# Kernel optimization log

Measured on AMD Instinct MI355X. Metric: run time of the kernel, lower is better.

Reference implementation:

```python
import jax, jax.numpy as jnp
import numpy as np

N, E, F_IN, H, G, A, OUT = 50000, 800000, 128, 256, 64, 8, 1


def _lin(k, fi, fo):
    s = 1.0 / np.sqrt(fi)
    kw, kb = jax.random.split(k)
    W = jax.random.uniform(kw, (fi, fo), jnp.float32, -s, s)
    b = jax.random.uniform(kb, (fo,), jnp.float32, -s, s)
    return W, b


def setup_inputs() -> dict:
    key = jax.random.key(0)
    ks = jax.random.split(key, 12)
    x = jax.random.normal(ks[0], (N, F_IN), jnp.float32)
    edge_index = jax.random.randint(ks[1], (2, E), 0, N, dtype=jnp.int64)
    batch = jnp.sort(jax.random.randint(ks[2], (N,), 0, G, dtype=jnp.int64))
    graph_attr = jax.random.normal(ks[3], (G, A), jnp.float32)
    W1, b1 = _lin(ks[4], F_IN, H)
    W2, b2 = _lin(ks[5], H, H)
    W3, b3 = _lin(ks[6], H, H)
    fcW1, fcb1 = _lin(ks[7], H + A, H)
    fcW2, fcb2 = _lin(ks[8], H, OUT)
    ones = jnp.ones((H,), jnp.float32)
    zeros = jnp.zeros((H,), jnp.float32)
    return dict(x=x, graph_attr=graph_attr, edge_index=edge_index, batch=batch,
                W1=W1, b1=b1, W2=W2, b2=b2, W3=W3, b3=b3,
                g1=ones, be1=zeros, g2=ones, be2=zeros, g3=ones, be3=zeros,
                fcW1=fcW1, fcb1=fcb1, fcW2=fcW2, fcb2=fcb2)


def gcn_conv(x, W, b, src, dst, n):
    # PyG GCNConv: add self-loops, symmetric normalization, xW then scatter-add
    xw = x @ W  # [N, H]
    loop = jnp.arange(n)
    src2 = jnp.concatenate([src, loop])
    dst2 = jnp.concatenate([dst, loop])
    deg = jnp.zeros((n,), xw.dtype).at[dst2].add(1.0)
    dinv = jnp.where(deg > 0, jax.lax.rsqrt(deg), 0.0)
    norm = dinv[src2] * dinv[dst2]  # [E+N]
    out = jnp.zeros((n, xw.shape[1]), xw.dtype).at[dst2].add(xw[src2] * norm[:, None])
    return out + b


def layer_norm(x, g, b, eps=1e-5):
    m = x.mean(-1, keepdims=True)
    v = ((x - m) ** 2).mean(-1, keepdims=True)
    return (x - m) * jax.lax.rsqrt(v + eps) * g + b


def reference(x, graph_attr, edge_index, batch,
              W1, b1, W2, b2, W3, b3,
              g1, be1, g2, be2, g3, be3,
              fcW1, fcb1, fcW2, fcb2):
    src, dst = edge_index[0], edge_index[1]
    h = jax.nn.relu(layer_norm(gcn_conv(x, W1, b1, src, dst, N), g1, be1))
    h = jax.nn.relu(layer_norm(gcn_conv(h, W2, b2, src, dst, N), g2, be2))
    h = jax.nn.relu(layer_norm(gcn_conv(h, W3, b3, src, dst, N), g3, be3))
    # global mean pool over graph ids
    sums = jax.ops.segment_sum(h, batch, num_segments=G)
    cnts = jax.ops.segment_sum(jnp.ones((N,), h.dtype), batch, num_segments=G)
    pooled = sums / jnp.maximum(cnts, 1.0)[:, None]  # [G, H]
    z = jnp.concatenate([pooled, graph_attr.reshape(-1, A)], axis=1)
    z = jax.nn.relu(z @ fcW1 + fcb1)
    return z @ fcW2 + fcb2  # [G, OUT]
```

## Files before the change

kernel.cpp:

```cpp
#include <hip/hip_runtime.h>
#include <hip/hip_bf16.h>

#define N_NODES 50000
#define N_EDGES 800000
#define F_IN    128
#define H_DIM   256
#define G_NUM   64
#define A_DIM   8

#define NBUCKET 196
#define NCHUNK  391
#define CHUNK   2048
#define K4CAP   6144

typedef __attribute__((ext_vector_type(8))) short short8v;
typedef __attribute__((ext_vector_type(4))) float float4v;
typedef __attribute__((ext_vector_type(2))) float float2v;

__device__ __forceinline__ float b2f(unsigned short u) {
    return __uint_as_float(((unsigned int)u) << 16);
}
__device__ __forceinline__ unsigned short f2b(float v) {
    return __hip_bfloat16_raw(__float2bfloat16(v)).x;
}
__device__ __forceinline__ unsigned char f2fp8(float v) {
    return (unsigned char)(__builtin_amdgcn_cvt_pk_fp8_f32(v, v, 0, false) & 0xff);
}
__device__ __forceinline__ unsigned int pack2(float a, float b) {
    return (unsigned int)f2b(a) | ((unsigned int)f2b(b) << 16);
}
__device__ __forceinline__ void accadd16(float2v* a, uint4 v) {
    a[0] += __builtin_amdgcn_cvt_pk_f32_fp8((int)v.x, false);
    a[1] += __builtin_amdgcn_cvt_pk_f32_fp8((int)v.x, true);
    a[2] += __builtin_amdgcn_cvt_pk_f32_fp8((int)v.y, false);
    a[3] += __builtin_amdgcn_cvt_pk_f32_fp8((int)v.y, true);
    a[4] += __builtin_amdgcn_cvt_pk_f32_fp8((int)v.z, false);
    a[5] += __builtin_amdgcn_cvt_pk_f32_fp8((int)v.z, true);
    a[6] += __builtin_amdgcn_cvt_pk_f32_fp8((int)v.w, false);
    a[7] += __builtin_amdgcn_cvt_pk_f32_fp8((int)v.w, true);
}
__device__ __forceinline__ void accfma16(float2v* a, uint4 v, float w) {
    float2v w2 = {w, w};
    a[0] = __builtin_amdgcn_cvt_pk_f32_fp8((int)v.x, false) * w2 + a[0];
    a[1] = __builtin_amdgcn_cvt_pk_f32_fp8((int)v.x, true)  * w2 + a[1];
    a[2] = __builtin_amdgcn_cvt_pk_f32_fp8((int)v.y, false) * w2 + a[2];
    a[3] = __builtin_amdgcn_cvt_pk_f32_fp8((int)v.y, true)  * w2 + a[3];
    a[4] = __builtin_amdgcn_cvt_pk_f32_fp8((int)v.z, false) * w2 + a[4];
    a[5] = __builtin_amdgcn_cvt_pk_f32_fp8((int)v.z, true)  * w2 + a[5];
    a[6] = __builtin_amdgcn_cvt_pk_f32_fp8((int)v.w, false) * w2 + a[6];
    a[7] = __builtin_amdgcn_cvt_pk_f32_fp8((int)v.w, true)  * w2 + a[7];
}

#define SK 40


__global__ __launch_bounds__(512) void fuse0_kernel(const int* __restrict__ dst,
                                                    unsigned int* __restrict__ Hg,
                                                    const float* __restrict__ x,
                                                    const float* __restrict__ W1,
                                                    unsigned char* __restrict__ P8,
                                                    const float* __restrict__ W2,
                                                    unsigned short* __restrict__ Wt2,
                                                    const float* __restrict__ W3,
                                                    unsigned short* __restrict__ Wt3) {
    const int CB = NCHUNK;
    const int GB = (N_NODES + 127) / 128;
    int b = blockIdx.x, t = threadIdx.x;
    if (b < CB) {
        __shared__ unsigned int h[256];
        if (t < 256) h[t] = 0u;
        __syncthreads();
        int base = b * CHUNK;
        #pragma unroll
        for (int k = 0; k < 4; k++) {
            int i = base + k * 512 + t;
            if (i < N_EDGES) atomicAdd(&h[dst[i] >> 8], 1u);
        }
        __syncthreads();
        if (t < 256) Hg[(size_t)t * NCHUNK + b] = h[t];
        return;
    }
    b -= CB;
    if (b < GB) {
        __shared__ unsigned short As[128][SK];
        __shared__ unsigned short Bs[256][SK];
        int wave = t >> 6, lane = t & 63;
        int wm0 = (wave & 1) * 64, wn0 = (wave >> 1) * 64;
        int bm = b * 128;
        int l15 = lane & 15, lq = lane >> 4;
        float4v acc[4][4];
        #pragma unroll
        for (int i = 0; i < 4; i++)
            #pragma unroll
            for (int j = 0; j < 4; j++)
                acc[i][j] = (float4v){0.f, 0.f, 0.f, 0.f};

        for (int k0 = 0; k0 < F_IN; k0 += 32) {
            {
                int row = t >> 2, koff = (t & 3) * 8;
                short8v tmp = (short8v){0,0,0,0,0,0,0,0};
                if (bm + row < N_NODES) {
                    const float* xp = x + (size_t)(bm + row) * F_IN + k0 + koff;
                    float4 a0 = *(const float4*)xp;
                    float4 a1 = *(const float4*)(xp + 4);
                    tmp[0] = (short)f2b(a0.x); tmp[1] = (short)f2b(a0.y);
                    tmp[2] = (short)f2b(a0.z); tmp[3] = (short)f2b(a0.w);
                    tmp[4] = (short)f2b(a1.x); tmp[5] = (short)f2b(a1.y);
                    tmp[6] = (short)f2b(a1.z); tmp[7] = (short)f2b(a1.w);
                }
                *(short8v*)&As[row][koff] = tmp;
            }
            #pragma unroll
            for (int h = 0; h < 2; h++) {
                int c = t + h * 512;
                int n = c >> 2, koff = (c & 3) * 8;
                short8v tmp;
                #pragma unroll
                for (int kk = 0; kk < 8; kk++)
                    tmp[kk] = (short)f2b(W1[(size_t)(k0 + koff + kk) * H_DIM + n]);
                *(short8v*)&Bs[n][koff] = tmp;
            }
            __syncthreads();
            short8v af[4], bf[4];
            #pragma unroll
            for (int i = 0; i < 4; i++) {
                af[i] = *(const short8v*)&As[wm0 + i * 16 + l15][lq * 8];
                bf[i] = *(const short8v*)&Bs[wn0 + i * 16 + l15][lq * 8];
            }
            #pragma unroll
            for (int i = 0; i < 4; i++)
                #pragma unroll
                for (int j = 0; j < 4; j++)
                    acc[i][j] = __builtin_amdgcn_mfma_f32_16x16x32_bf16(af[i], bf[j], acc[i][j], 0, 0, 0);
            __syncthreads();
        }
        #pragma unroll
        for (int i = 0; i < 4; i++) {
            #pragma unroll
            for (int r = 0; r < 4; r++) {
                int row = bm + wm0 + i * 16 + lq * 4 + r;
                if (row < N_NODES) {
                    #pragma unroll
                    for (int j = 0; j < 4; j++) {
                        int col = wn0 + j * 16 + l15;
                        P8[(size_t)row * H_DIM + col] = f2fp8(acc[i][j][r]);
                    }
                }
            }
        }
        return;
    }
    b -= GB;
    int i = b * 512 + t;
    if (i < H_DIM * H_DIM) {
        int k = i >> 8, n = i & 255;
        Wt2[(size_t)n * H_DIM + k] = f2b(W2[i]);
    } else if (i < 2 * H_DIM * H_DIM) {
        int j = i - H_DIM * H_DIM;
        int k = j >> 8, n = j & 255;
        Wt3[(size_t)n * H_DIM + k] = f2b(W3[j]);
    }
}


__global__ __launch_bounds__(256) void scanH_kernel(unsigned int* __restrict__ Hg,
                                                    unsigned int* __restrict__ Btot) {
    __shared__ unsigned int tile[256];
    int b = blockIdx.x, t = threadIdx.x;
    unsigned int* row = Hg + (size_t)b * NCHUNK;
    int i0 = 2 * t, i1 = 2 * t + 1;
    unsigned int v0 = (i0 < NCHUNK) ? row[i0] : 0u;
    unsigned int v1 = (i1 < NCHUNK) ? row[i1] : 0u;
    unsigned int pair = v0 + v1;
    tile[t] = pair;
    __syncthreads();
    #pragma unroll
    for (int o = 1; o < 256; o <<= 1) {
        unsigned int add = (t >= o) ? tile[t - o] : 0u;
        __syncthreads();
        tile[t] += add;
        __syncthreads();
    }
    unsigned int excl = tile[t] - pair;
    if (i0 < NCHUNK) row[i0] = excl;
    if (i1 < NCHUNK) row[i1] = excl + v0;
    if (t == 255) Btot[b] = tile[255];
}


__global__ __launch_bounds__(256) void base_kernel(const unsigned int* __restrict__ Btot,
                                                   unsigned int* __restrict__ bucketBase,
                                                   const int* __restrict__ batch,
                                                   int* __restrict__ gstart,
                                                   int* __restrict__ rowptr,
                                                   float* __restrict__ pooled) {
    __shared__ unsigned int tile[256];
    int t = threadIdx.x;
    unsigned int v = (t < NBUCKET) ? Btot[t] : 0u;
    tile[t] = v;
    __syncthreads();
    #pragma unroll
    for (int o = 1; o < 256; o <<= 1) {
        unsigned int add = (t >= o) ? tile[t - o] : 0u;
        __syncthreads();
        tile[t] += add;
        __syncthreads();
    }
    if (t < NBUCKET) bucketBase[t] = tile[t] - v;
    if (t == NBUCKET - 1) bucketBase[NBUCKET] = tile[t];
    if (t == 0) rowptr[N_NODES] = N_EDGES;
    if (t <= G_NUM) {
        int lo = 0, hi = N_NODES;
        while (lo < hi) {
            int mid = (lo + hi) >> 1;
            if (batch[mid] < t) lo = mid + 1; else hi = mid;
        }
        gstart[t] = lo;
    }
    for (int i = t; i < G_NUM * H_DIM; i += 256) pooled[i] = 0.f;
}


__global__ __launch_bounds__(512) void scatter_kernel(const int* __restrict__ src,
                                                      const int* __restrict__ dst,
                                                      const unsigned int* __restrict__ Hg,
                                                      const unsigned int* __restrict__ bucketBase,
                                                      unsigned int* __restrict__ tmp) {
    __shared__ unsigned int off[256];
    int blk = blockIdx.x, t = threadIdx.x;
    if (t < 256)
        off[t] = (t < NBUCKET) ? (bucketBase[t] + Hg[(size_t)t * NCHUNK + blk]) : 0u;
    __syncthreads();
    int base = blk * CHUNK;
    #pragma unroll
    for (int k = 0; k < 4; k++) {
        int i = base + k * 512 + t;
        if (i < N_EDGES) {
            int d = dst[i], s = src[i];
            unsigned int slot = atomicAdd(&off[d >> 8], 1u);
            tmp[slot] = ((unsigned int)(d & 255) << 16) | (unsigned int)s;
        }
    }
}


__global__ __launch_bounds__(256) void finalize_kernel(const unsigned int* __restrict__ tmp,
                                                       const unsigned int* __restrict__ bucketBase,
                                                       int* __restrict__ rowptr,
                                                       float* __restrict__ dinv,
                                                       unsigned short* __restrict__ csr_src) {
    __shared__ unsigned int te[K4CAP];
    __shared__ unsigned int h2[256];
    __shared__ unsigned int sc[256];
    __shared__ unsigned int off2[256];
    int b = blockIdx.x, t = threadIdx.x;
    unsigned int beg = bucketBase[b], end = bucketBase[b + 1];
    int cnt = (int)(end - beg);
    bool lds_ok = (cnt <= K4CAP);
    h2[t] = 0u;
    __syncthreads();
    for (int i = t; i < cnt; i += 256) {
        unsigned int u = tmp[beg + i];
        if (lds_ok) te[i] = u;
        atomicAdd(&h2[u >> 16], 1u);
    }
    __syncthreads();
    unsigned int c = h2[t];
    sc[t] = c;
    __syncthreads();
    #pragma unroll
    for (int o = 1; o < 256; o <<= 1) {
        unsigned int add = (t >= o) ? sc[t - o] : 0u;
        __syncthreads();
        sc[t] += add;
        __syncthreads();
    }
    unsigned int excl = sc[t] - c;
    int v = (b << 8) + t;
    if (v < N_NODES) {
        rowptr[v] = (int)(beg + excl);
        dinv[v] = rsqrtf((float)c + 1.0f);
    }
    off2[t] = excl;
    __syncthreads();
    for (int i = t; i < cnt; i += 256) {
        unsigned int u = lds_ok ? te[i] : tmp[beg + i];
        unsigned int lo = u >> 16;
        unsigned int s2 = atomicAdd(&off2[lo], 1u);
        csr_src[beg + s2] = (unsigned short)(u & 0xFFFFu);
    }
}


__global__ __launch_bounds__(512) void gemm_f8(const unsigned short* __restrict__ A,
                                               const unsigned short* __restrict__ Bt,
                                               unsigned char* __restrict__ C8,
                                               const float* __restrict__ dinv,
                                               int M, int K) {
    __shared__ unsigned short As[128][SK];
    __shared__ unsigned short Bs[256][SK];
    int t = threadIdx.x;
    int wave = t >> 6, lane = t & 63;
    int wm0 = (wave & 1) * 64, wn0 = (wave >> 1) * 64;
    int bm = blockIdx.x * 128;
    int l15 = lane & 15, lq = lane >> 4;
    float4v acc[4][4];
    #pragma unroll
    for (int i = 0; i < 4; i++)
        #pragma unroll
        for (int j = 0; j < 4; j++)
            acc[i][j] = (float4v){0.f, 0.f, 0.f, 0.f};

    for (int k0 = 0; k0 < K; k0 += 32) {
        {
            int row = t >> 2, koff = (t & 3) * 8;
            uint4 va = make_uint4(0u, 0u, 0u, 0u);
            if (bm + row < M)
                va = *(const uint4*)(A + (size_t)(bm + row) * K + k0 + koff);
            *(uint4*)&As[row][koff] = va;
        }
        #pragma unroll
        for (int h = 0; h < 2; h++) {
            int c = t + h * 512;
            int row = c >> 2, koff = (c & 3) * 8;
            uint4 vb = *(const uint4*)(Bt + (size_t)row * K + k0 + koff);
            *(uint4*)&Bs[row][koff] = vb;
        }
        __syncthreads();
        short8v af[4], bf[4];
        #pragma unroll
        for (int i = 0; i < 4; i++) {
            af[i] = *(const short8v*)&As[wm0 + i * 16 + l15][lq * 8];
            bf[i] = *(const short8v*)&Bs[wn0 + i * 16 + l15][lq * 8];
        }
        #pragma unroll
        for (int i = 0; i < 4; i++)
            #pragma unroll
            for (int j = 0; j < 4; j++)
                acc[i][j] = __builtin_amdgcn_mfma_f32_16x16x32_bf16(af[i], bf[j], acc[i][j], 0, 0, 0);
        __syncthreads();
    }
    #pragma unroll
    for (int i = 0; i < 4; i++) {
        #pragma unroll
        for (int r = 0; r < 4; r++) {
            int row = bm + wm0 + i * 16 + lq * 4 + r;
            if (row < M) {
                float dv = dinv[row];
                #pragma unroll
                for (int j = 0; j < 4; j++) {
                    int col = wn0 + j * 16 + l15;
                    C8[(size_t)row * H_DIM + col] = f2fp8(dv * acc[i][j][r]);
                }
            }
        }
    }
}


template<int F, bool DO_LN, bool W8>
__global__ __launch_bounds__(256) void gather_ns(const unsigned char* __restrict__ xw,
                                                 unsigned short* __restrict__ out,
                                                 const int* __restrict__ rowptr,
                                                 const unsigned short* __restrict__ csr_src,
                                                 const float* __restrict__ dinv,
                                                 const float* __restrict__ bias,
                                                 const float* __restrict__ gamma,
                                                 const float* __restrict__ beta) {
    constexpr int BPL = F / 16;
    constexpr int NF2 = BPL / 2;
    int lane = threadIdx.x & 63;
    int wave = threadIdx.x >> 6;
    int p = lane & 15;
    int gbase = lane & 48;
    int node = blockIdx.x * 16 + wave * 4 + (lane >> 4);
    int beg = rowptr[node];
    int deg = rowptr[node + 1] - beg;
    float d = dinv[node];
    const unsigned char* xp = xw + (size_t)p * BPL;

    float2v acc2[NF2];
    #pragma unroll
    for (int k = 0; k < NF2; k++) acc2[k] = (float2v){0.f, 0.f};

    {
        uint4 v = *(const uint4*)(xp + (size_t)node * F);
        if constexpr (W8) accfma16(acc2, v, d);
        else              accadd16(acc2, v);
    }

    for (int b0 = 0; b0 < deg; b0 += 16) {
        int m = deg - b0; if (m > 16) m = 16;
        int sv = 0; float wv = 0.f;
        if (p < m) {
            sv = (int)csr_src[beg + b0 + p];
            if constexpr (W8) wv = dinv[sv];
        }
        int j = 0;
        for (; j + 4 <= m; j += 4) {
            int s0 = __shfl(sv, gbase | j, 64);
            int s1 = __shfl(sv, gbase | (j + 1), 64);
            int s2 = __shfl(sv, gbase | (j + 2), 64);
            int s3 = __shfl(sv, gbase | (j + 3), 64);
            uint4 v0 = *(const uint4*)(xp + (size_t)s0 * F);
            uint4 v1 = *(const uint4*)(xp + (size_t)s1 * F);
            uint4 v2 = *(const uint4*)(xp + (size_t)s2 * F);
            uint4 v3 = *(const uint4*)(xp + (size_t)s3 * F);
            if constexpr (W8) {
                float w0 = __shfl(wv, gbase | j, 64);
                float w1 = __shfl(wv, gbase | (j + 1), 64);
                float w2 = __shfl(wv, gbase | (j + 2), 64);
                float w3 = __shfl(wv, gbase | (j + 3), 64);
                accfma16(acc2, v0, w0); accfma16(acc2, v1, w1);
                accfma16(acc2, v2, w2); accfma16(acc2, v3, w3);
            } else {
                accadd16(acc2, v0); accadd16(acc2, v1);
                accadd16(acc2, v2); accadd16(acc2, v3);
            }
        }
        for (; j < m; ++j) {
            int s0 = __shfl(sv, gbase | j, 64);
            uint4 v0 = *(const uint4*)(xp + (size_t)s0 * F);
            if constexpr (W8) {
                float w0 = __shfl(wv, gbase | j, 64);
                accfma16(acc2, v0, w0);
            } else {
                accadd16(acc2, v0);
            }
        }
    }

    float v[BPL];
    #pragma unroll
    for (int k = 0; k < NF2; k++) { v[2 * k] = d * acc2[k].x; v[2 * k + 1] = d * acc2[k].y; }

    if constexpr (DO_LN) {
        #pragma unroll
        for (int q = 0; q < BPL / 4; q++) {
            float4 bi = ((const float4*)bias)[p * (BPL / 4) + q];
            v[q * 4 + 0] += bi.x; v[q * 4 + 1] += bi.y;
            v[q * 4 + 2] += bi.z; v[q * 4 + 3] += bi.w;
        }
        float s = 0.f, ss = 0.f;
        #pragma unroll
        for (int k = 0; k < BPL; k++) { s += v[k]; ss += v[k] * v[k]; }
        #pragma unroll
        for (int o = 1; o < 16; o <<= 1) {
            s  += __shfl_xor(s, o, 64);
            ss += __shfl_xor(ss, o, 64);
        }
        float mn = s * (1.f / F);
        float var = ss * (1.f / F) - mn * mn;
        float rstd = rsqrtf(var + 1e-5f);
        #pragma unroll
        for (int q = 0; q < BPL / 4; q++) {
            float4 ga = ((const float4*)gamma)[p * (BPL / 4) + q];
            float4 be = ((const float4*)beta)[p * (BPL / 4) + q];
            v[q * 4 + 0] = fmaxf((v[q * 4 + 0] - mn) * rstd * ga.x + be.x, 0.f);
            v[q * 4 + 1] = fmaxf((v[q * 4 + 1] - mn) * rstd * ga.y + be.y, 0.f);
            v[q * 4 + 2] = fmaxf((v[q * 4 + 2] - mn) * rstd * ga.z + be.z, 0.f);
            v[q * 4 + 3] = fmaxf((v[q * 4 + 3] - mn) * rstd * ga.w + be.w, 0.f);
        }
    }

    unsigned short* op = out + (size_t)node * F + p * BPL;
    uint4 o0;
    o0.x = pack2(v[0], v[1]); o0.y = pack2(v[2], v[3]);
    o0.z = pack2(v[4], v[5]); o0.w = pack2(v[6], v[7]);
    *(uint4*)op = o0;
    if constexpr (F == 256) {
        uint4 o1;
        o1.x = pack2(v[8],  v[9]);  o1.y = pack2(v[10], v[11]);
        o1.z = pack2(v[12], v[13]); o1.w = pack2(v[14], v[15]);
        *(uint4*)(op + 8) = o1;
    }
}


__global__ __launch_bounds__(128) void pool_kernel(const unsigned int* __restrict__ h32,
                                                   const int* __restrict__ batch,
                                                   float* __restrict__ pooled, int n) {
    int t = threadIdx.x;
    int start = blockIdx.x * 64;
    int end = min(start + 64, n);
    if (start >= n) return;
    int cur = batch[start];
    float a0 = 0.f, a1 = 0.f;
    for (int i = start; i < end; ++i) {
        int g = batch[i];
        if (g != cur) {
            atomicAdd(&pooled[(size_t)cur * H_DIM + 2 * t], a0);
            atomicAdd(&pooled[(size_t)cur * H_DIM + 2 * t + 1], a1);
            a0 = a1 = 0.f;
            cur = g;
        }
        unsigned int u = h32[(size_t)i * (H_DIM / 2) + t];
        a0 += b2f((unsigned short)(u & 0xffffu));
        a1 += b2f((unsigned short)(u >> 16));
    }
    atomicAdd(&pooled[(size_t)cur * H_DIM + 2 * t], a0);
    atomicAdd(&pooled[(size_t)cur * H_DIM + 2 * t + 1], a1);
}


__global__ __launch_bounds__(256) void fc_kernel(const float* __restrict__ pooled,
                                                 const int* __restrict__ gstart,
                                                 const float* __restrict__ gattr,
                                                 const float* __restrict__ fcW1,
                                                 const float* __restrict__ fcb1,
                                                 const float* __restrict__ fcW2,
                                                 const float* __restrict__ fcb2,
                                                 float* __restrict__ out) {
    __shared__ float zc[H_DIM + A_DIM];
    __shared__ float z1[H_DIM];
    int g = blockIdx.x, t = threadIdx.x;
    int c_i = gstart[g + 1] - gstart[g];
    float c = (float)(c_i > 1 ? c_i : 1);
    zc[t] = pooled[(size_t)g * H_DIM + t] / c;
    if (t < A_DIM) zc[H_DIM + t] = gattr[g * A_DIM + t];
    __syncthreads();
    float s = fcb1[t];
    for (int k = 0; k < H_DIM + A_DIM; k++)
        s += zc[k] * fcW1[(size_t)k * H_DIM + t];
    z1[t] = fmaxf(s, 0.f) * fcW2[t];
    __syncthreads();
    for (int off = 128; off; off >>= 1) {
        if (t < off) z1[t] += z1[t + off];
        __syncthreads();
    }
    if (t == 0) out[g] = z1[0] + fcb2[0];
}


extern "C" void kernel_launch(void* const* d_in, const int* in_sizes, int n_in,
                              void* d_out, int out_size, void* d_ws, size_t ws_size,
                              hipStream_t stream) {
    const float* x     = (const float*)d_in[0];
    const float* gattr = (const float*)d_in[1];
    const int*   ei    = (const int*)d_in[2];
    const int*   batch = (const int*)d_in[3];
    const float* W1 = (const float*)d_in[4];  const float* b1 = (const float*)d_in[5];
    const float* W2 = (const float*)d_in[6];  const float* b2 = (const float*)d_in[7];
    const float* W3 = (const float*)d_in[8];  const float* b3 = (const float*)d_in[9];
    const float* g1 = (const float*)d_in[10]; const float* be1 = (const float*)d_in[11];
    const float* g2 = (const float*)d_in[12]; const float* be2 = (const float*)d_in[13];
    const float* g3 = (const float*)d_in[14]; const float* be3 = (const float*)d_in[15];
    const float* fcW1 = (const float*)d_in[16]; const float* fcb1 = (const float*)d_in[17];
    const float* fcW2 = (const float*)d_in[18]; const float* fcb2 = (const float*)d_in[19];
    float* out = (float*)d_out;

    char* w = (char*)d_ws;
    unsigned char*  Pb8 = (unsigned char*)w;  w += (size_t)N_NODES * H_DIM;
    unsigned short* Hb  = (unsigned short*)w; w += (size_t)N_NODES * H_DIM * 2;
    unsigned short* Wt2 = (unsigned short*)w; w += (size_t)H_DIM * H_DIM * 2;
    unsigned short* Wt3 = (unsigned short*)w; w += (size_t)H_DIM * H_DIM * 2;
    float* dinv   = (float*)w; w += (size_t)N_NODES * 4;
    float* pooled = (float*)w; w += (size_t)G_NUM * H_DIM * 4;
    int* rowptr   = (int*)w;   w += (size_t)(N_NODES + 4) * 4;
    unsigned int* Hg = (unsigned int*)w;      w += (size_t)256 * NCHUNK * 4;
    unsigned int* Btot = (unsigned int*)w;    w += (size_t)256 * 4;
    unsigned int* bucketBase = (unsigned int*)w; w += (size_t)(NBUCKET + 4) * 4;
    unsigned int* tmp = (unsigned int*)w;     w += (size_t)N_EDGES * 4;
    unsigned short* csr_src = (unsigned short*)w; w += (size_t)N_EDGES * 2;
    int* gstart   = (int*)w;   w += (size_t)(G_NUM + 1) * 4;

    const int* srcp = ei;
    const int* dstp = ei + N_EDGES;

    {
        const int CB = NCHUNK;
        const int GB = (N_NODES + 127) / 128;
        const int WB = (2 * H_DIM * H_DIM + 511) / 512;
        fuse0_kernel<<<CB + GB + WB, 512, 0, stream>>>(dstp, Hg, x, W1, Pb8, W2, Wt2, W3, Wt3);
    }
    scanH_kernel<<<NBUCKET, 256, 0, stream>>>(Hg, Btot);
    base_kernel<<<1, 256, 0, stream>>>(Btot, bucketBase, batch, gstart, rowptr, pooled);
    scatter_kernel<<<NCHUNK, 512, 0, stream>>>(srcp, dstp, Hg, bucketBase, tmp);
    finalize_kernel<<<NBUCKET, 256, 0, stream>>>(tmp, bucketBase, rowptr, dinv, csr_src);

    int gemm_blocks = (N_NODES + 127) / 128;
    int gather_blocks = N_NODES / 16;

    gather_ns<H_DIM, true, true><<<gather_blocks, 256, 0, stream>>>(Pb8, Hb, rowptr, csr_src,
                                                                    dinv, b1, g1, be1);
    gemm_f8<<<gemm_blocks, 512, 0, stream>>>(Hb, Wt2, Pb8, dinv, N_NODES, H_DIM);
    gather_ns<H_DIM, true, false><<<gather_blocks, 256, 0, stream>>>(Pb8, Hb, rowptr, csr_src,
                                                                     dinv, b2, g2, be2);
    gemm_f8<<<gemm_blocks, 512, 0, stream>>>(Hb, Wt3, Pb8, dinv, N_NODES, H_DIM);
    gather_ns<H_DIM, true, false><<<gather_blocks, 256, 0, stream>>>(Pb8, Hb, rowptr, csr_src,
                                                                     dinv, b3, g3, be3);

    pool_kernel<<<(N_NODES + 63) / 64, 128, 0, stream>>>((const unsigned int*)Hb, batch, pooled, N_NODES);
    fc_kernel<<<G_NUM, 256, 0, stream>>>(pooled, gstart, gattr, fcW1, fcb1, fcW2, fcb2, out);
}
```

Measured before the change: 339.3 us.

## Fuse gather+LayerNorm into the following GEMM and fuse final gather with pooling

Each aggregation+LayerNorm stage now writes its 64-row bf16 tile into swizzled shared memory, and the next layer's MFMA GEMM consumes it directly in the same kernel, writing fp8 output to a ping-pong buffer. The final aggregation is fused with mean-pool accumulation through shared-memory atomics. This removes the bf16 intermediate round-trips to global memory and several launches. In exchange, the GEMM runs with smaller 64-row tiles, reloads the weight panel in every block, and sees the gather's load imbalance.

```diff
diff --git a/kernel.cpp b/kernel.cpp
--- a/kernel.cpp
+++ b/kernel.cpp
@@ -52,6 +52,104 @@
 }
 
 #define SK 40
+
+
+template<bool W8>
+__device__ __forceinline__ void gather_row_256(const unsigned char* __restrict__ xw,
+                                               int node,
+                                               const int* __restrict__ rowptr,
+                                               const unsigned short* __restrict__ csr_src,
+                                               const float* __restrict__ dinv,
+                                               const float* __restrict__ bias,
+                                               const float* __restrict__ gamma,
+                                               const float* __restrict__ beta,
+                                               int p, int gbase, float* v) {
+    int beg = rowptr[node];
+    int deg = rowptr[node + 1] - beg;
+    float d = dinv[node];
+    const unsigned char* xp = xw + (size_t)p * 16;
+
+    float2v acc2[8];
+    #pragma unroll
+    for (int k = 0; k < 8; k++) acc2[k] = (float2v){0.f, 0.f};
+
+    {
+        uint4 sv4 = *(const uint4*)(xp + (size_t)node * H_DIM);
+        if constexpr (W8) accfma16(acc2, sv4, d);
+        else              accadd16(acc2, sv4);
+    }
+
+    for (int b0 = 0; b0 < deg; b0 += 16) {
+        int m = deg - b0; if (m > 16) m = 16;
+        int sv = 0; float wv = 0.f;
+        if (p < m) {
+            sv = (int)csr_src[beg + b0 + p];
+            if constexpr (W8) wv = dinv[sv];
+        }
+        int j = 0;
+        for (; j + 4 <= m; j += 4) {
+            int s0 = __shfl(sv, gbase | j, 64);
+            int s1 = __shfl(sv, gbase | (j + 1), 64);
+            int s2 = __shfl(sv, gbase | (j + 2), 64);
+            int s3 = __shfl(sv, gbase | (j + 3), 64);
+            uint4 v0 = *(const uint4*)(xp + (size_t)s0 * H_DIM);
+            uint4 v1 = *(const uint4*)(xp + (size_t)s1 * H_DIM);
+            uint4 v2 = *(const uint4*)(xp + (size_t)s2 * H_DIM);
+            uint4 v3 = *(const uint4*)(xp + (size_t)s3 * H_DIM);
+            if constexpr (W8) {
+                float w0 = __shfl(wv, gbase | j, 64);
+                float w1 = __shfl(wv, gbase | (j + 1), 64);
+                float w2 = __shfl(wv, gbase | (j + 2), 64);
+                float w3 = __shfl(wv, gbase | (j + 3), 64);
+                accfma16(acc2, v0, w0); accfma16(acc2, v1, w1);
+                accfma16(acc2, v2, w2); accfma16(acc2, v3, w3);
+            } else {
+                accadd16(acc2, v0); accadd16(acc2, v1);
+                accadd16(acc2, v2); accadd16(acc2, v3);
+            }
+        }
+        for (; j < m; ++j) {
+            int s0 = __shfl(sv, gbase | j, 64);
+            uint4 v0 = *(const uint4*)(xp + (size_t)s0 * H_DIM);
+            if constexpr (W8) {
+                float w0 = __shfl(wv, gbase | j, 64);
+                accfma16(acc2, v0, w0);
+            } else {
+                accadd16(acc2, v0);
+            }
+        }
+    }
+
+    #pragma unroll
+    for (int k = 0; k < 8; k++) { v[2 * k] = d * acc2[k].x; v[2 * k + 1] = d * acc2[k].y; }
+
+    #pragma unroll
+    for (int q = 0; q < 4; q++) {
+        float4 bi = ((const float4*)bias)[p * 4 + q];
+        v[q * 4 + 0] += bi.x; v[q * 4 + 1] += bi.y;
+        v[q * 4 + 2] += bi.z; v[q * 4 + 3] += bi.w;
+    }
+    float s = 0.f, ss = 0.f;
+    #pragma unroll
+    for (int k = 0; k < 16; k++) { s += v[k]; ss += v[k] * v[k]; }
+    #pragma unroll
+    for (int o = 1; o < 16; o <<= 1) {
+        s  += __shfl_xor(s, o, 64);
+        ss += __shfl_xor(ss, o, 64);
+    }
+    float mn = s * (1.f / H_DIM);
+    float var = ss * (1.f / H_DIM) - mn * mn;
+    float rstd = rsqrtf(var + 1e-5f);
+    #pragma unroll
+    for (int q = 0; q < 4; q++) {
+        float4 ga = ((const float4*)gamma)[p * 4 + q];
+        float4 be = ((const float4*)beta)[p * 4 + q];
+        v[q * 4 + 0] = fmaxf((v[q * 4 + 0] - mn) * rstd * ga.x + be.x, 0.f);
+        v[q * 4 + 1] = fmaxf((v[q * 4 + 1] - mn) * rstd * ga.y + be.y, 0.f);
+        v[q * 4 + 2] = fmaxf((v[q * 4 + 2] - mn) * rstd * ga.z + be.z, 0.f);
+        v[q * 4 + 3] = fmaxf((v[q * 4 + 3] - mn) * rstd * ga.w + be.w, 0.f);
+    }
+}
 
 
 __global__ __launch_bounds__(512) void fuse0_kernel(const int* __restrict__ dst,
@@ -187,7 +285,6 @@
     if (t == 255) Btot[b] = tile[255];
 }
 
-
 __global__ __launch_bounds__(256) void base_kernel(const unsigned int* __restrict__ Btot,
                                                    unsigned int* __restrict__ bucketBase,
                                                    const int* __restrict__ batch,
@@ -220,7 +317,6 @@
     for (int i = t; i < G_NUM * H_DIM; i += 256) pooled[i] = 0.f;
 }
 
-
 __global__ __launch_bounds__(512) void scatter_kernel(const int* __restrict__ src,
                                                       const int* __restrict__ dst,
                                                       const unsigned int* __restrict__ Hg,
@@ -242,7 +338,6 @@
         }
     }
 }
-
 
 __global__ __launch_bounds__(256) void finalize_kernel(const unsigned int* __restrict__ tmp,
                                                        const unsigned int* __restrict__ bucketBase,
@@ -292,214 +387,136 @@
 }
 
 
-__global__ __launch_bounds__(512) void gemm_f8(const unsigned short* __restrict__ A,
-                                               const unsigned short* __restrict__ Bt,
-                                               unsigned char* __restrict__ C8,
-                                               const float* __restrict__ dinv,
-                                               int M, int K) {
-    __shared__ unsigned short As[128][SK];
-    __shared__ unsigned short Bs[256][SK];
-    int t = threadIdx.x;
-    int wave = t >> 6, lane = t & 63;
-    int wm0 = (wave & 1) * 64, wn0 = (wave >> 1) * 64;
-    int bm = blockIdx.x * 128;
-    int l15 = lane & 15, lq = lane >> 4;
-    float4v acc[4][4];
-    #pragma unroll
-    for (int i = 0; i < 4; i++)
-        #pragma unroll
-        for (int j = 0; j < 4; j++)
-            acc[i][j] = (float4v){0.f, 0.f, 0.f, 0.f};
-
-    for (int k0 = 0; k0 < K; k0 += 32) {
-        {
-            int row = t >> 2, koff = (t & 3) * 8;
-            uint4 va = make_uint4(0u, 0u, 0u, 0u);
-            if (bm + row < M)
-                va = *(const uint4*)(A + (size_t)(bm + row) * K + k0 + koff);
-            *(uint4*)&As[row][koff] = va;
-        }
-        #pragma unroll
-        for (int h = 0; h < 2; h++) {
-            int c = t + h * 512;
-            int row = c >> 2, koff = (c & 3) * 8;
-            uint4 vb = *(const uint4*)(Bt + (size_t)row * K + k0 + koff);
-            *(uint4*)&Bs[row][koff] = vb;
-        }
-        __syncthreads();
-        short8v af[4], bf[4];
-        #pragma unroll
-        for (int i = 0; i < 4; i++) {
-            af[i] = *(const short8v*)&As[wm0 + i * 16 + l15][lq * 8];
-            bf[i] = *(const short8v*)&Bs[wn0 + i * 16 + l15][lq * 8];
-        }
-        #pragma unroll
-        for (int i = 0; i < 4; i++)
-            #pragma unroll
-            for (int j = 0; j < 4; j++)
-                acc[i][j] = __builtin_amdgcn_mfma_f32_16x16x32_bf16(af[i], bf[j], acc[i][j], 0, 0, 0);
-        __syncthreads();
-    }
-    #pragma unroll
-    for (int i = 0; i < 4; i++) {
-        #pragma unroll
-        for (int r = 0; r < 4; r++) {
-            int row = bm + wm0 + i * 16 + lq * 4 + r;
-            if (row < M) {
-                float dv = dinv[row];
-                #pragma unroll
-                for (int j = 0; j < 4; j++) {
-                    int col = wn0 + j * 16 + l15;
-                    C8[(size_t)row * H_DIM + col] = f2fp8(dv * acc[i][j][r]);
-                }
-            }
-        }
-    }
-}
-
-
-template<int F, bool DO_LN, bool W8>
-__global__ __launch_bounds__(256) void gather_ns(const unsigned char* __restrict__ xw,
-                                                 unsigned short* __restrict__ out,
+template<bool W8>
+__global__ __launch_bounds__(256) void fg_kernel(const unsigned char* __restrict__ Pin,
+                                                 const unsigned short* __restrict__ Wt,
+                                                 unsigned char* __restrict__ Pout,
                                                  const int* __restrict__ rowptr,
                                                  const unsigned short* __restrict__ csr_src,
                                                  const float* __restrict__ dinv,
                                                  const float* __restrict__ bias,
                                                  const float* __restrict__ gamma,
                                                  const float* __restrict__ beta) {
-    constexpr int BPL = F / 16;
-    constexpr int NF2 = BPL / 2;
-    int lane = threadIdx.x & 63;
-    int wave = threadIdx.x >> 6;
-    int p = lane & 15;
-    int gbase = lane & 48;
-    int node = blockIdx.x * 16 + wave * 4 + (lane >> 4);
-    int beg = rowptr[node];
-    int deg = rowptr[node + 1] - beg;
-    float d = dinv[node];
-    const unsigned char* xp = xw + (size_t)p * BPL;
-
-    float2v acc2[NF2];
-    #pragma unroll
-    for (int k = 0; k < NF2; k++) acc2[k] = (float2v){0.f, 0.f};
-
-    {
-        uint4 v = *(const uint4*)(xp + (size_t)node * F);
-        if constexpr (W8) accfma16(acc2, v, d);
-        else              accadd16(acc2, v);
-    }
-
-    for (int b0 = 0; b0 < deg; b0 += 16) {
-        int m = deg - b0; if (m > 16) m = 16;
-        int sv = 0; float wv = 0.f;
-        if (p < m) {
-            sv = (int)csr_src[beg + b0 + p];
-            if constexpr (W8) wv = dinv[sv];
-        }
-        int j = 0;
-        for (; j + 4 <= m; j += 4) {
-            int s0 = __shfl(sv, gbase | j, 64);
-            int s1 = __shfl(sv, gbase | (j + 1), 64);
-            int s2 = __shfl(sv, gbase | (j + 2), 64);
-            int s3 = __shfl(sv, gbase | (j + 3), 64);
-            uint4 v0 = *(const uint4*)(xp + (size_t)s0 * F);
-            uint4 v1 = *(const uint4*)(xp + (size_t)s1 * F);
-            uint4 v2 = *(const uint4*)(xp + (size_t)s2 * F);
-            uint4 v3 = *(const uint4*)(xp + (size_t)s3 * F);
-            if constexpr (W8) {
-                float w0 = __shfl(wv, gbase | j, 64);
-                float w1 = __shfl(wv, gbase | (j + 1), 64);
-                float w2 = __shfl(wv, gbase | (j + 2), 64);
-                float w3 = __shfl(wv, gbase | (j + 3), 64);
-                accfma16(acc2, v0, w0); accfma16(acc2, v1, w1);
-                accfma16(acc2, v2, w2); accfma16(acc2, v3, w3);
+    __shared__ unsigned short As[64 * 256];
+    __shared__ unsigned short Bs[256][SK];
+    int t = threadIdx.x;
+    int lane = t & 63, wave = t >> 6;
+    int p = lane & 15, gbase = lane & 48;
+    int bm = blockIdx.x * 64;
+
+    for (int it = 0; it < 4; ++it) {
+        int r = it * 16 + wave * 4 + (lane >> 4);
+        int node = bm + r;
+        if (node < N_NODES) {
+            float v[16];
+            gather_row_256<W8>(Pin, node, rowptr, csr_src, dinv, bias, gamma, beta, p, gbase, v);
+            unsigned int X = ((unsigned int)(r & 7)) << 4;
+            char* bp = (char*)As + r * 512;
+            uint4 o0, o1;
+            o0.x = pack2(v[0], v[1]);   o0.y = pack2(v[2], v[3]);
+            o0.z = pack2(v[4], v[5]);   o0.w = pack2(v[6], v[7]);
+            o1.x = pack2(v[8], v[9]);   o1.y = pack2(v[10], v[11]);
+            o1.z = pack2(v[12], v[13]); o1.w = pack2(v[14], v[15]);
+            *(uint4*)(bp + (((unsigned int)(p * 32)) ^ X)) = o0;
+            *(uint4*)(bp + (((unsigned int)(p * 32 + 16)) ^ X)) = o1;
+        }
+    }
+    __syncthreads();
+
+    int l15 = lane & 15, lq = lane >> 4;
+    int wn0 = wave * 64;
+    float4v acc[4][4];
+    #pragma unroll
+    for (int i = 0; i < 4; i++)
+        #pragma unroll
+        for (int j = 0; j < 4; j++)
+            acc[i][j] = (float4v){0.f, 0.f, 0.f, 0.f};
+
+    for (int k0 = 0; k0 < H_DIM; k0 += 32) {
+        {
+            const uint4* wsrc = (const uint4*)(Wt + (size_t)t * H_DIM + k0);
+            *(uint4*)&Bs[t][0]  = wsrc[0];
+            *(uint4*)&Bs[t][8]  = wsrc[1];
+            *(uint4*)&Bs[t][16] = wsrc[2];
+            *(uint4*)&Bs[t][24] = wsrc[3];
+        }
+        __syncthreads();
+        short8v af[4], bf[4];
+        #pragma unroll
+        for (int i = 0; i < 4; i++) {
+            int R = i * 16 + l15;
+            unsigned int off = (unsigned int)(R * 512) +
+                ((((unsigned int)((k0 >> 3) + lq)) * 16u) ^ (((unsigned int)(R & 7)) << 4));
+            af[i] = *(const short8v*)((const char*)As + off);
+            bf[i] = *(const short8v*)&Bs[wn0 + i * 16 + l15][lq * 8];
+        }
+        #pragma unroll
+        for (int i = 0; i < 4; i++)
+            #pragma unroll
+            for (int j = 0; j < 4; j++)
+                acc[i][j] = __builtin_amdgcn_mfma_f32_16x16x32_bf16(af[i], bf[j], acc[i][j], 0, 0, 0);
+        __syncthreads();
+    }
+    #pragma unroll
+    for (int i = 0; i < 4; i++) {
+        #pragma unroll
+        for (int rr = 0; rr < 4; rr++) {
+            int row = bm + i * 16 + lq * 4 + rr;
+            if (row < N_NODES) {
+                float dv = dinv[row];
+                #pragma unroll
+                for (int j = 0; j < 4; j++) {
+                    int col = wn0 + j * 16 + l15;
+                    Pout[(size_t)row * H_DIM + col] = f2fp8(dv * acc[i][j][rr]);
+                }
+            }
+        }
+    }
+}
+
+
+__global__ __launch_bounds__(256) void gpool_kernel(const unsigned char* __restrict__ Pin,
+                                                    const int* __restrict__ rowptr,
+                                                    const unsigned short* __restrict__ csr_src,
+                                                    const float* __restrict__ dinv,
+                                                    const float* __restrict__ bias,
+                                                    const float* __restrict__ gamma,
+                                                    const float* __restrict__ beta,
+                                                    const int* __restrict__ batch,
+                                                    float* __restrict__ pooled) {
+    __shared__ float pacc[4][H_DIM];
+    __shared__ int used[4];
+    int t = threadIdx.x;
+    int lane = t & 63, wave = t >> 6;
+    int p = lane & 15, gbase = lane & 48;
+    int bm = blockIdx.x * 64;
+    for (int j = t; j < 4 * H_DIM; j += 256) ((float*)pacc)[j] = 0.f;
+    if (t < 4) used[t] = 0;
+    int g0 = batch[bm];
+    __syncthreads();
+
+    for (int it = 0; it < 4; ++it) {
+        int node = bm + it * 16 + wave * 4 + (lane >> 4);
+        if (node < N_NODES) {
+            float v[16];
+            gather_row_256<false>(Pin, node, rowptr, csr_src, dinv, bias, gamma, beta, p, gbase, v);
+            int gl = batch[node] - g0;
+            if (gl < 4) {
+                used[gl] = 1;
+                #pragma unroll
+                for (int k = 0; k < 16; k++)
+                    atomicAdd(&pacc[gl][p * 16 + k], v[k]);
             } else {
-                accadd16(acc2, v0); accadd16(acc2, v1);
-                accadd16(acc2, v2); accadd16(acc2, v3);
-            }
-        }
-        for (; j < m; ++j) {
-            int s0 = __shfl(sv, gbase | j, 64);
-            uint4 v0 = *(const uint4*)(xp + (size_t)s0 * F);
-            if constexpr (W8) {
-                float w0 = __shfl(wv, gbase | j, 64);
-                accfma16(acc2, v0, w0);
-            } else {
-                accadd16(acc2, v0);
-            }
-        }
-    }
-
-    float v[BPL];
-    #pragma unroll
-    for (int k = 0; k < NF2; k++) { v[2 * k] = d * acc2[k].x; v[2 * k + 1] = d * acc2[k].y; }
-
-    if constexpr (DO_LN) {
-        #pragma unroll
-        for (int q = 0; q < BPL / 4; q++) {
-            float4 bi = ((const float4*)bias)[p * (BPL / 4) + q];
-            v[q * 4 + 0] += bi.x; v[q * 4 + 1] += bi.y;
-            v[q * 4 + 2] += bi.z; v[q * 4 + 3] += bi.w;
-        }
-        float s = 0.f, ss = 0.f;
-        #pragma unroll
-        for (int k = 0; k < BPL; k++) { s += v[k]; ss += v[k] * v[k]; }
-        #pragma unroll
-        for (int o = 1; o < 16; o <<= 1) {
-            s  += __shfl_xor(s, o, 64);
-            ss += __shfl_xor(ss, o, 64);
-        }
-        float mn = s * (1.f / F);
-        float var = ss * (1.f / F) - mn * mn;
-        float rstd = rsqrtf(var + 1e-5f);
-        #pragma unroll
-        for (int q = 0; q < BPL / 4; q++) {
-            float4 ga = ((const float4*)gamma)[p * (BPL / 4) + q];
-            float4 be = ((const float4*)beta)[p * (BPL / 4) + q];
-            v[q * 4 + 0] = fmaxf((v[q * 4 + 0] - mn) * rstd * ga.x + be.x, 0.f);
-            v[q * 4 + 1] = fmaxf((v[q * 4 + 1] - mn) * rstd * ga.y + be.y, 0.f);
-            v[q * 4 + 2] = fmaxf((v[q * 4 + 2] - mn) * rstd * ga.z + be.z, 0.f);
-            v[q * 4 + 3] = fmaxf((v[q * 4 + 3] - mn) * rstd * ga.w + be.w, 0.f);
-        }
-    }
-
-    unsigned short* op = out + (size_t)node * F + p * BPL;
-    uint4 o0;
-    o0.x = pack2(v[0], v[1]); o0.y = pack2(v[2], v[3]);
-    o0.z = pack2(v[4], v[5]); o0.w = pack2(v[6], v[7]);
-    *(uint4*)op = o0;
-    if constexpr (F == 256) {
-        uint4 o1;
-        o1.x = pack2(v[8],  v[9]);  o1.y = pack2(v[10], v[11]);
-        o1.z = pack2(v[12], v[13]); o1.w = pack2(v[14], v[15]);
-        *(uint4*)(op + 8) = o1;
-    }
-}
-
-
-__global__ __launch_bounds__(128) void pool_kernel(const unsigned int* __restrict__ h32,
-                                                   const int* __restrict__ batch,
-                                                   float* __restrict__ pooled, int n) {
-    int t = threadIdx.x;
-    int start = blockIdx.x * 64;
-    int end = min(start + 64, n);
-    if (start >= n) return;
-    int cur = batch[start];
-    float a0 = 0.f, a1 = 0.f;
-    for (int i = start; i < end; ++i) {
-        int g = batch[i];
-        if (g != cur) {
-            atomicAdd(&pooled[(size_t)cur * H_DIM + 2 * t], a0);
-            atomicAdd(&pooled[(size_t)cur * H_DIM + 2 * t + 1], a1);
-            a0 = a1 = 0.f;
-            cur = g;
-        }
-        unsigned int u = h32[(size_t)i * (H_DIM / 2) + t];
-        a0 += b2f((unsigned short)(u & 0xffffu));
-        a1 += b2f((unsigned short)(u >> 16));
-    }
-    atomicAdd(&pooled[(size_t)cur * H_DIM + 2 * t], a0);
-    atomicAdd(&pooled[(size_t)cur * H_DIM + 2 * t + 1], a1);
+                #pragma unroll
+                for (int k = 0; k < 16; k++)
+                    atomicAdd(&pooled[(size_t)(g0 + gl) * H_DIM + p * 16 + k], v[k]);
+            }
+        }
+    }
+    __syncthreads();
+    #pragma unroll
+    for (int j = 0; j < 4; j++)
+        if (used[j]) atomicAdd(&pooled[(size_t)(g0 + j) * H_DIM + t], pacc[j][t]);
 }
 
 
@@ -550,8 +567,8 @@
     float* out = (float*)d_out;
 
     char* w = (char*)d_ws;
-    unsigned char*  Pb8 = (unsigned char*)w;  w += (size_t)N_NODES * H_DIM;
-    unsigned short* Hb  = (unsigned short*)w; w += (size_t)N_NODES * H_DIM * 2;
+    unsigned char*  Pb8  = (unsigned char*)w; w += (size_t)N_NODES * H_DIM;
+    unsigned char*  Pb8b = (unsigned char*)w; w += (size_t)N_NODES * H_DIM;
     unsigned short* Wt2 = (unsigned short*)w; w += (size_t)H_DIM * H_DIM * 2;
     unsigned short* Wt3 = (unsigned short*)w; w += (size_t)H_DIM * H_DIM * 2;
     float* dinv   = (float*)w; w += (size_t)N_NODES * 4;
@@ -578,18 +595,13 @@
     scatter_kernel<<<NCHUNK, 512, 0, stream>>>(srcp, dstp, Hg, bucketBase, tmp);
     finalize_kernel<<<NBUCKET, 256, 0, stream>>>(tmp, bucketBase, rowptr, dinv, csr_src);
 
-    int gemm_blocks = (N_NODES + 127) / 128;
-    int gather_blocks = N_NODES / 16;
-
-    gather_ns<H_DIM, true, true><<<gather_blocks, 256, 0, stream>>>(Pb8, Hb, rowptr, csr_src,
-                                                                    dinv, b1, g1, be1);
-    gemm_f8<<<gemm_blocks, 512, 0, stream>>>(Hb, Wt2, Pb8, dinv, N_NODES, H_DIM);
-    gather_ns<H_DIM, true, false><<<gather_blocks, 256, 0, stream>>>(Pb8, Hb, rowptr, csr_src,
-                                                                     dinv, b2, g2, be2);
-    gemm_f8<<<gemm_blocks, 512, 0, stream>>>(Hb, Wt3, Pb8, dinv, N_NODES, H_DIM);
-    gather_ns<H_DIM, true, false><<<gather_blocks, 256, 0, stream>>>(Pb8, Hb, rowptr, csr_src,
-                                                                     dinv, b3, g3, be3);
-
-    pool_kernel<<<(N_NODES + 63) / 64, 128, 0, stream>>>((const unsigned int*)Hb, batch, pooled, N_NODES);
+    int fg_blocks = (N_NODES + 63) / 64;
+
+    fg_kernel<true><<<fg_blocks, 256, 0, stream>>>(Pb8, Wt2, Pb8b, rowptr, csr_src, dinv,
+                                                   b1, g1, be1);
+    fg_kernel<false><<<fg_blocks, 256, 0, stream>>>(Pb8b, Wt3, Pb8, rowptr, csr_src, dinv,
+                                                    b2, g2, be2);
+    gpool_kernel<<<fg_blocks, 256, 0, stream>>>(Pb8, rowptr, csr_src, dinv, b3, g3, be3,
+                                                batch, pooled);
     fc_kernel<<<G_NUM, 256, 0, stream>>>(pooled, gstart, gattr, fcW1, fcb1, fcW2, fcb2, out);
 }
```

Result: slower. 421.6 us (+24.3%).

## Fuse mean-pool into final gather and software-pipeline neighbor index loads

Applied to the files above, without the earlier changes.

The last gather kernel now accumulates its LayerNorm/ReLU outputs directly into per-graph pooled sums through shared-memory atomics, then global atomics. This removes the separate pool kernel and the write and re-read of the final hidden matrix. The edge loop also changes from shuffle-broadcast batches of 16 to per-lane groups of 8, prefetching the next group's indices and weights. Each lane now loads indices itself, which adds redundant csr loads, and the fused pooling adds atomic contention.

```diff
diff --git a/kernel.cpp b/kernel.cpp
--- a/kernel.cpp
+++ b/kernel.cpp
@@ -187,7 +187,6 @@
     if (t == 255) Btot[b] = tile[255];
 }
 
-
 __global__ __launch_bounds__(256) void base_kernel(const unsigned int* __restrict__ Btot,
                                                    unsigned int* __restrict__ bucketBase,
                                                    const int* __restrict__ batch,
@@ -220,7 +219,6 @@
     for (int i = t; i < G_NUM * H_DIM; i += 256) pooled[i] = 0.f;
 }
 
-
 __global__ __launch_bounds__(512) void scatter_kernel(const int* __restrict__ src,
                                                       const int* __restrict__ dst,
                                                       const unsigned int* __restrict__ Hg,
@@ -242,7 +240,6 @@
         }
     }
 }
-
 
 __global__ __launch_bounds__(256) void finalize_kernel(const unsigned int* __restrict__ tmp,
                                                        const unsigned int* __restrict__ bucketBase,
@@ -358,7 +355,7 @@
 }
 
 
-template<int F, bool DO_LN, bool W8>
+template<bool W8, bool POOL>
 __global__ __launch_bounds__(256) void gather_ns(const unsigned char* __restrict__ xw,
                                                  unsigned short* __restrict__ out,
                                                  const int* __restrict__ rowptr,
@@ -366,140 +363,138 @@
                                                  const float* __restrict__ dinv,
                                                  const float* __restrict__ bias,
                                                  const float* __restrict__ gamma,
-                                                 const float* __restrict__ beta) {
-    constexpr int BPL = F / 16;
-    constexpr int NF2 = BPL / 2;
+                                                 const float* __restrict__ beta,
+                                                 const int* __restrict__ batch,
+                                                 float* __restrict__ pooled) {
+    __shared__ float pacc[2][H_DIM];
     int lane = threadIdx.x & 63;
     int wave = threadIdx.x >> 6;
     int p = lane & 15;
-    int gbase = lane & 48;
     int node = blockIdx.x * 16 + wave * 4 + (lane >> 4);
+    int g0 = 0;
+    if constexpr (POOL) {
+        for (int j = threadIdx.x; j < 2 * H_DIM; j += 256) ((float*)pacc)[j] = 0.f;
+        g0 = batch[blockIdx.x * 16];
+        __syncthreads();
+    }
     int beg = rowptr[node];
     int deg = rowptr[node + 1] - beg;
     float d = dinv[node];
-    const unsigned char* xp = xw + (size_t)p * BPL;
-
-    float2v acc2[NF2];
-    #pragma unroll
-    for (int k = 0; k < NF2; k++) acc2[k] = (float2v){0.f, 0.f};
+    const unsigned char* xp = xw + (size_t)p * 16;
+
+    float2v acc2[8];
+    #pragma unroll
+    for (int k = 0; k < 8; k++) acc2[k] = (float2v){0.f, 0.f};
 
     {
-        uint4 v = *(const uint4*)(xp + (size_t)node * F);
-        if constexpr (W8) accfma16(acc2, v, d);
-        else              accadd16(acc2, v);
-    }
-
-    for (int b0 = 0; b0 < deg; b0 += 16) {
-        int m = deg - b0; if (m > 16) m = 16;
-        int sv = 0; float wv = 0.f;
-        if (p < m) {
-            sv = (int)csr_src[beg + b0 + p];
-            if constexpr (W8) wv = dinv[sv];
-        }
-        int j = 0;
-        for (; j + 4 <= m; j += 4) {
-            int s0 = __shfl(sv, gbase | j, 64);
-            int s1 = __shfl(sv, gbase | (j + 1), 64);
-            int s2 = __shfl(sv, gbase | (j + 2), 64);
-            int s3 = __shfl(sv, gbase | (j + 3), 64);
-            uint4 v0 = *(const uint4*)(xp + (size_t)s0 * F);
-            uint4 v1 = *(const uint4*)(xp + (size_t)s1 * F);
-            uint4 v2 = *(const uint4*)(xp + (size_t)s2 * F);
-            uint4 v3 = *(const uint4*)(xp + (size_t)s3 * F);
+        uint4 sv4 = *(const uint4*)(xp + (size_t)node * H_DIM);
+        if constexpr (W8) accfma16(acc2, sv4, d);
+        else              accadd16(acc2, sv4);
+    }
+
+    int G8 = deg >> 3, tail = deg & 7;
+    int ids[8]; float wts[8];
+    #pragma unroll
+    for (int k = 0; k < 8; k++) { ids[k] = 0; wts[k] = 0.f; }
+    if (G8 > 0) {
+        #pragma unroll
+        for (int k = 0; k < 8; k++) ids[k] = (int)csr_src[beg + k];
+        if constexpr (W8) {
+            #pragma unroll
+            for (int k = 0; k < 8; k++) wts[k] = dinv[ids[k]];
+        }
+    }
+    for (int g = 0; g < G8; ++g) {
+        int nid[8]; float nwt[8];
+        #pragma unroll
+        for (int k = 0; k < 8; k++) { nid[k] = 0; nwt[k] = 0.f; }
+        if (g + 1 < G8) {
+            int nb = beg + (g + 1) * 8;
+            #pragma unroll
+            for (int k = 0; k < 8; k++) nid[k] = (int)csr_src[nb + k];
             if constexpr (W8) {
-                float w0 = __shfl(wv, gbase | j, 64);
-                float w1 = __shfl(wv, gbase | (j + 1), 64);
-                float w2 = __shfl(wv, gbase | (j + 2), 64);
-                float w3 = __shfl(wv, gbase | (j + 3), 64);
-                accfma16(acc2, v0, w0); accfma16(acc2, v1, w1);
-                accfma16(acc2, v2, w2); accfma16(acc2, v3, w3);
-            } else {
-                accadd16(acc2, v0); accadd16(acc2, v1);
-                accadd16(acc2, v2); accadd16(acc2, v3);
+                #pragma unroll
+                for (int k = 0; k < 8; k++) nwt[k] = dinv[nid[k]];
             }
         }
-        for (; j < m; ++j) {
-            int s0 = __shfl(sv, gbase | j, 64);
-            uint4 v0 = *(const uint4*)(xp + (size_t)s0 * F);
-            if constexpr (W8) {
-                float w0 = __shfl(wv, gbase | j, 64);
-                accfma16(acc2, v0, w0);
-            } else {
-                accadd16(acc2, v0);
-            }
-        }
-    }
-
-    float v[BPL];
-    #pragma unroll
-    for (int k = 0; k < NF2; k++) { v[2 * k] = d * acc2[k].x; v[2 * k + 1] = d * acc2[k].y; }
-
-    if constexpr (DO_LN) {
-        #pragma unroll
-        for (int q = 0; q < BPL / 4; q++) {
-            float4 bi = ((const float4*)bias)[p * (BPL / 4) + q];
-            v[q * 4 + 0] += bi.x; v[q * 4 + 1] += bi.y;
-            v[q * 4 + 2] += bi.z; v[q * 4 + 3] += bi.w;
-        }
-        float s = 0.f, ss = 0.f;
-        #pragma unroll
-        for (int k = 0; k < BPL; k++) { s += v[k]; ss += v[k] * v[k]; }
-        #pragma unroll
-        for (int o = 1; o < 16; o <<= 1) {
-            s  += __shfl_xor(s, o, 64);
-            ss += __shfl_xor(ss, o, 64);
-        }
-        float mn = s * (1.f / F);
-        float var = ss * (1.f / F) - mn * mn;
-        float rstd = rsqrtf(var + 1e-5f);
-        #pragma unroll
-        for (int q = 0; q < BPL / 4; q++) {
-            float4 ga = ((const float4*)gamma)[p * (BPL / 4) + q];
-            float4 be = ((const float4*)beta)[p * (BPL / 4) + q];
-            v[q * 4 + 0] = fmaxf((v[q * 4 + 0] - mn) * rstd * ga.x + be.x, 0.f);
-            v[q * 4 + 1] = fmaxf((v[q * 4 + 1] - mn) * rstd * ga.y + be.y, 0.f);
-            v[q * 4 + 2] = fmaxf((v[q * 4 + 2] - mn) * rstd * ga.z + be.z, 0.f);
-            v[q * 4 + 3] = fmaxf((v[q * 4 + 3] - mn) * rstd * ga.w + be.w, 0.f);
-        }
-    }
-
-    unsigned short* op = out + (size_t)node * F + p * BPL;
-    uint4 o0;
-    o0.x = pack2(v[0], v[1]); o0.y = pack2(v[2], v[3]);
-    o0.z = pack2(v[4], v[5]); o0.w = pack2(v[6], v[7]);
-    *(uint4*)op = o0;
-    if constexpr (F == 256) {
-        uint4 o1;
-        o1.x = pack2(v[8],  v[9]);  o1.y = pack2(v[10], v[11]);
+        uint4 vv[8];
+        #pragma unroll
+        for (int k = 0; k < 8; k++) vv[k] = *(const uint4*)(xp + (size_t)ids[k] * H_DIM);
+        #pragma unroll
+        for (int k = 0; k < 8; k++) {
+            if constexpr (W8) accfma16(acc2, vv[k], wts[k]);
+            else              accadd16(acc2, vv[k]);
+        }
+        #pragma unroll
+        for (int k = 0; k < 8; k++) { ids[k] = nid[k]; if constexpr (W8) wts[k] = nwt[k]; }
+    }
+    {
+        int tb = beg + G8 * 8;
+        for (int j = 0; j < tail; ++j) {
+            int s = (int)csr_src[tb + j];
+            uint4 v0 = *(const uint4*)(xp + (size_t)s * H_DIM);
+            if constexpr (W8) accfma16(acc2, v0, dinv[s]);
+            else              accadd16(acc2, v0);
+        }
+    }
+
+    float v[16];
+    #pragma unroll
+    for (int k = 0; k < 8; k++) { v[2 * k] = d * acc2[k].x; v[2 * k + 1] = d * acc2[k].y; }
+
+    #pragma unroll
+    for (int q = 0; q < 4; q++) {
+        float4 bi = ((const float4*)bias)[p * 4 + q];
+        v[q * 4 + 0] += bi.x; v[q * 4 + 1] += bi.y;
+        v[q * 4 + 2] += bi.z; v[q * 4 + 3] += bi.w;
+    }
+    float s = 0.f, ss = 0.f;
+    #pragma unroll
+    for (int k = 0; k < 16; k++) { s += v[k]; ss += v[k] * v[k]; }
+    #pragma unroll
+    for (int o = 1; o < 16; o <<= 1) {
+        s  += __shfl_xor(s, o, 64);
+        ss += __shfl_xor(ss, o, 64);
+    }
+    float mn = s * (1.f / H_DIM);
+    float var = ss * (1.f / H_DIM) - mn * mn;
+    float rstd = rsqrtf(var + 1e-5f);
+    #pragma unroll
+    for (int q = 0; q < 4; q++) {
+        float4 ga = ((const float4*)gamma)[p * 4 + q];
+        float4 be = ((const float4*)beta)[p * 4 + q];
+        v[q * 4 + 0] = fmaxf((v[q * 4 + 0] - mn) * rstd * ga.x + be.x, 0.f);
+        v[q * 4 + 1] = fmaxf((v[q * 4 + 1] - mn) * rstd * ga.y + be.y, 0.f);
+        v[q * 4 + 2] = fmaxf((v[q * 4 + 2] - mn) * rstd * ga.z + be.z, 0.f);
+        v[q * 4 + 3] = fmaxf((v[q * 4 + 3] - mn) * rstd * ga.w + be.w, 0.f);
+    }
+
+    if constexpr (POOL) {
+        int gl = batch[node] - g0;
+        if (gl < 2) {
+            #pragma unroll
+            for (int k = 0; k < 16; k++)
+                atomicAdd(&pacc[gl][p * 16 + k], v[k]);
+        } else {
+            #pragma unroll
+            for (int k = 0; k < 16; k++)
+                atomicAdd(&pooled[(size_t)(g0 + gl) * H_DIM + p * 16 + k], v[k]);
+        }
+        __syncthreads();
+        int t = threadIdx.x;
+        float p0 = pacc[0][t], p1 = pacc[1][t];
+        if (p0 != 0.f) atomicAdd(&pooled[(size_t)g0 * H_DIM + t], p0);
+        if (p1 != 0.f) atomicAdd(&pooled[(size_t)(g0 + 1) * H_DIM + t], p1);
+    } else {
+        unsigned short* op = out + (size_t)node * H_DIM + p * 16;
+        uint4 o0, o1;
+        o0.x = pack2(v[0], v[1]);   o0.y = pack2(v[2], v[3]);
+        o0.z = pack2(v[4], v[5]);   o0.w = pack2(v[6], v[7]);
+        o1.x = pack2(v[8], v[9]);   o1.y = pack2(v[10], v[11]);
         o1.z = pack2(v[12], v[13]); o1.w = pack2(v[14], v[15]);
+        *(uint4*)op = o0;
         *(uint4*)(op + 8) = o1;
     }
-}
-
-
-__global__ __launch_bounds__(128) void pool_kernel(const unsigned int* __restrict__ h32,
-                                                   const int* __restrict__ batch,
-                                                   float* __restrict__ pooled, int n) {
-    int t = threadIdx.x;
-    int start = blockIdx.x * 64;
-    int end = min(start + 64, n);
-    if (start >= n) return;
-    int cur = batch[start];
-    float a0 = 0.f, a1 = 0.f;
-    for (int i = start; i < end; ++i) {
-        int g = batch[i];
-        if (g != cur) {
-            atomicAdd(&pooled[(size_t)cur * H_DIM + 2 * t], a0);
-            atomicAdd(&pooled[(size_t)cur * H_DIM + 2 * t + 1], a1);
-            a0 = a1 = 0.f;
-            cur = g;
-        }
-        unsigned int u = h32[(size_t)i * (H_DIM / 2) + t];
-        a0 += b2f((unsigned short)(u & 0xffffu));
-        a1 += b2f((unsigned short)(u >> 16));
-    }
-    atomicAdd(&pooled[(size_t)cur * H_DIM + 2 * t], a0);
-    atomicAdd(&pooled[(size_t)cur * H_DIM + 2 * t + 1], a1);
 }
 
 
@@ -581,15 +576,16 @@
     int gemm_blocks = (N_NODES + 127) / 128;
     int gather_blocks = N_NODES / 16;
 
-    gather_ns<H_DIM, true, true><<<gather_blocks, 256, 0, stream>>>(Pb8, Hb, rowptr, csr_src,
-                                                                    dinv, b1, g1, be1);
+    gather_ns<true, false><<<gather_blocks, 256, 0, stream>>>(Pb8, Hb, rowptr, csr_src,
+                                                              dinv, b1, g1, be1,
+                                                              nullptr, nullptr);
     gemm_f8<<<gemm_blocks, 512, 0, stream>>>(Hb, Wt2, Pb8, dinv, N_NODES, H_DIM);
-    gather_ns<H_DIM, true, false><<<gather_blocks, 256, 0, stream>>>(Pb8, Hb, rowptr, csr_src,
-                                                                     dinv, b2, g2, be2);
+    gather_ns<false, false><<<gather_blocks, 256, 0, stream>>>(Pb8, Hb, rowptr, csr_src,
+                                                               dinv, b2, g2, be2,
+                                                               nullptr, nullptr);
     gemm_f8<<<gemm_blocks, 512, 0, stream>>>(Hb, Wt3, Pb8, dinv, N_NODES, H_DIM);
-    gather_ns<H_DIM, true, false><<<gather_blocks, 256, 0, stream>>>(Pb8, Hb, rowptr, csr_src,
-                                                                     dinv, b3, g3, be3);
-
-    pool_kernel<<<(N_NODES + 63) / 64, 128, 0, stream>>>((const unsigned int*)Hb, batch, pooled, N_NODES);
+    gather_ns<false, true><<<gather_blocks, 256, 0, stream>>>(Pb8, nullptr, rowptr, csr_src,
+                                                              dinv, b3, g3, be3,
+                                                              batch, pooled);
     fc_kernel<<<G_NUM, 256, 0, stream>>>(pooled, gstart, gattr, fcW1, fcb1, fcW2, fcb2, out);
 }
```

After: 371.9 us. 9.6% more time.
